# Optimization experiments

Measured on AMD Instinct MI355X. Metric: run time of the kernel, lower is better.

## Reference

```python
import jax, jax.numpy as jnp
import numpy as np

B, T, V, E, U = 32, 512, 8000, 256, 512


def _lstm(x, mask, Wk, Wr, b):
    """Keras-semantics masked LSTM. x:[B,T,D], mask:[B,T] bool -> [B,T,U].
    At masked steps the state is not updated and the output carries the
    previous hidden state (Keras K.rnn default, zero_output_for_mask=False)."""
    xW = jnp.einsum('btd,dk->btk', x, Wk) + b  # precompute input projections [B,T,4U]
    units = Wr.shape[0]

    def step(carry, inp):
        h, c = carry
        xw, m = inp  # xw:[B,4U], m:[B]
        z = xw + h @ Wr
        i, f, g, o = jnp.split(z, 4, axis=-1)  # Keras gate order i,f,c,o
        c_new = jax.nn.sigmoid(f) * c + jax.nn.sigmoid(i) * jnp.tanh(g)
        h_new = jax.nn.sigmoid(o) * jnp.tanh(c_new)
        m2 = m[:, None]
        h_new = jnp.where(m2, h_new, h)
        c_new = jnp.where(m2, c_new, c)
        return (h_new, c_new), h_new

    h0 = jnp.zeros((x.shape[0], units), x.dtype)
    _, ys = jax.lax.scan(step, (h0, h0), (jnp.swapaxes(xW, 0, 1), mask.T))
    return jnp.swapaxes(ys, 0, 1)


def _bidir(x, mask, kf, rf, bf, kb, rb, bb):
    fwd = _lstm(x, mask, kf, rf, bf)
    bwd = _lstm(x[:, ::-1], mask[:, ::-1], kb, rb, bb)[:, ::-1]
    return jnp.concatenate([fwd, bwd], axis=-1)


def setup_inputs() -> dict:
    key = jax.random.key(0)
    ks = jax.random.split(key, 12)
    s = 0.05  # glorot-ish scale for stability through tanh/sigmoid
    return {
        'tokens': jax.random.randint(ks[0], (B, T), 0, V, dtype=jnp.int32),
        'emb': jax.random.normal(ks[1], (V, E), jnp.float32) * s,
        'k1f': jax.random.normal(ks[2], (E, 4 * U), jnp.float32) * s,
        'r1f': jax.random.normal(ks[3], (U, 4 * U), jnp.float32) * s,
        'b1f': jnp.zeros((4 * U,), jnp.float32),
        'k1b': jax.random.normal(ks[4], (E, 4 * U), jnp.float32) * s,
        'r1b': jax.random.normal(ks[5], (U, 4 * U), jnp.float32) * s,
        'b1b': jnp.zeros((4 * U,), jnp.float32),
        'k2f': jax.random.normal(ks[6], (2 * U, 4 * U), jnp.float32) * s,
        'r2f': jax.random.normal(ks[7], (U, 4 * U), jnp.float32) * s,
        'b2f': jnp.zeros((4 * U,), jnp.float32),
        'k2b': jax.random.normal(ks[8], (2 * U, 4 * U), jnp.float32) * s,
        'r2b': jax.random.normal(ks[9], (U, 4 * U), jnp.float32) * s,
        'b2b': jnp.zeros((4 * U,), jnp.float32),
        'wd': jax.random.normal(ks[10], (2 * U, V), jnp.float32) * s,
        'bd': jnp.zeros((V,), jnp.float32),
    }


def reference(tokens, emb, k1f, r1f, b1f, k1b, r1b, b1b,
              k2f, r2f, b2f, k2b, r2b, b2b, wd, bd):
    mask = tokens != 0  # Embedding(mask_zero=True)
    x = emb[tokens]  # [B,T,E]
    h1 = _bidir(x, mask, k1f, r1f, b1f, k1b, r1b, b1b)  # [B,T,2U]; Dropout is identity at inference
    h2 = _bidir(h1, mask, k2f, r2f, b2f, k2b, r2b, b2b)  # [B,T,2U]
    logits = jnp.einsum('btd,dv->btv', h2, wd) + bd  # [B,T,V]
    return logits
```

## Files before the change

### kernel.cpp

```cpp
#include <hip/hip_runtime.h>
#include <hip/hip_bf16.h>
#include <stdint.h>

#define B_   32
#define T_   512
#define V_   8000
#define E_   256
#define U_   512
#define BT_  (B_*T_)
#define G4_  (4*U_)
#define GWG  32
#define UPW  (U_/GWG)

typedef unsigned short ushort_t;
typedef __attribute__((ext_vector_type(8))) short   short8;
typedef __attribute__((ext_vector_type(4))) float   floatx4;

__device__ __forceinline__ float bf2f(ushort_t u) {
    union { unsigned int i; float f; } v; v.i = ((unsigned int)u) << 16; return v.f;
}
__device__ __forceinline__ ushort_t f2bf(float f) {
    union { float f; unsigned int i; } v; v.f = f;
    unsigned int r = v.i + 0x7fffu + ((v.i >> 16) & 1u);
    return (ushort_t)(r >> 16);
}
__device__ __forceinline__ float sigmoidf_(float x) { return 1.0f / (1.0f + __expf(-x)); }
__device__ __forceinline__ float tanhf_(float x) {
    float ax = fabsf(x);
    float e  = __expf(-2.0f * ax);
    float r  = (1.0f - e) / (1.0f + e);
    return copysignf(r, x);
}

__device__ __forceinline__ void stg_h_sc1(ushort_t* p, unsigned int v) {
    asm volatile("global_store_short %0, %1, off sc0 sc1"
                 :: "v"(p), "v"(v) : "memory");
}
template<int OFFB>
__device__ __forceinline__ short8 ldg_h_sc1(const ushort_t* p) {
    short8 r;
    asm volatile("global_load_dwordx4 %0, %1, off offset:%2 sc0 sc1"
                 : "=&v"(r) : "v"(p), "i"(OFFB));
    return r;
}

__global__ void embed_kernel(const int* __restrict__ tokens,
                             const float* __restrict__ emb,
                             ushort_t* __restrict__ x)
{
    int row = blockIdx.x * 4 + (threadIdx.x >> 6);
    int col = (threadIdx.x & 63) * 4;
    int tok = tokens[row];
    const float4 v = *(const float4*)(emb + (size_t)tok * E_ + col);
    ushort_t* dst = x + (size_t)row * E_ + col;
    dst[0] = f2bf(v.x); dst[1] = f2bf(v.y); dst[2] = f2bf(v.z); dst[3] = f2bf(v.w);
}

__global__ void transpose_f32_bf16(const float* __restrict__ in,
                                   ushort_t* __restrict__ out, int R, int C)
{
    __shared__ ushort_t tile[32][33];
    int c0 = blockIdx.x * 32, r0 = blockIdx.y * 32;
    int r = threadIdx.x >> 3;
    int c4 = (threadIdx.x & 7) * 4;
    const float* src = in + (size_t)(r0 + r) * C + c0 + c4;
    #pragma unroll
    for (int i = 0; i < 4; ++i) tile[r][c4 + i] = f2bf(src[i]);
    __syncthreads();
    ushort_t* dst = out + (size_t)(c0 + r) * R + r0 + c4;
    #pragma unroll
    for (int i = 0; i < 4; ++i) dst[i] = tile[c4 + i][r];
}

template <int MODE>
__global__ __launch_bounds__(256)
void gemm_bt(const ushort_t* __restrict__ A,
             const ushort_t* __restrict__ BT,
             const float* __restrict__ bias,
             void* __restrict__ Cv,
             int M, int Nd, int K)
{
    const int tid = threadIdx.x, lane = tid & 63, wave = tid >> 6;
    const int wm = wave >> 1, wn = wave & 1;
    const int m0 = blockIdx.x * 128;
    const int n0 = blockIdx.y * 128;
    __shared__ __align__(16) ushort_t As[128 * 32];
    __shared__ __align__(16) ushort_t Bs[128 * 32];
    floatx4 acc[4][4];
    #pragma unroll
    for (int i = 0; i < 4; ++i)
        #pragma unroll
        for (int j = 0; j < 4; ++j) acc[i][j] = (floatx4){0.f, 0.f, 0.f, 0.f};

    const int lr = lane >> 2;
    const int lk = (lane & 3) * 8;
    const int rowL = wave * 32 + lr;
    const int ra0 = m0 + rowL;
    int rb0 = n0 + rowL;      if (rb0 > Nd - 1) rb0 = Nd - 1;
    int rb1 = n0 + rowL + 16; if (rb1 > Nd - 1) rb1 = Nd - 1;

    for (int k0 = 0; k0 < K; k0 += 32) {
        uint4 a0 = *(const uint4*)(A  + (size_t)ra0        * K + k0 + lk);
        uint4 a1 = *(const uint4*)(A  + (size_t)(ra0 + 16) * K + k0 + lk);
        uint4 b0 = *(const uint4*)(BT + (size_t)rb0        * K + k0 + lk);
        uint4 b1 = *(const uint4*)(BT + (size_t)rb1        * K + k0 + lk);
        __syncthreads();
        *(uint4*)(As + (rowL     ) * 32 + lk) = a0;
        *(uint4*)(As + (rowL + 16) * 32 + lk) = a1;
        *(uint4*)(Bs + (rowL     ) * 32 + lk) = b0;
        *(uint4*)(Bs + (rowL + 16) * 32 + lk) = b1;
        __syncthreads();
        short8 af[4], bw[4];
        #pragma unroll
        for (int i = 0; i < 4; ++i)
            af[i] = *(const short8*)(As + (wm * 64 + i * 16 + (lane & 15)) * 32 + (lane >> 4) * 8);
        #pragma unroll
        for (int j = 0; j < 4; ++j)
            bw[j] = *(const short8*)(Bs + (wn * 64 + j * 16 + (lane & 15)) * 32 + (lane >> 4) * 8);
        #pragma unroll
        for (int i = 0; i < 4; ++i)
            #pragma unroll
            for (int j = 0; j < 4; ++j)
                acc[i][j] = __builtin_amdgcn_mfma_f32_16x16x32_bf16(af[i], bw[j], acc[i][j], 0, 0, 0);
    }
    #pragma unroll
    for (int j = 0; j < 4; ++j) {
        int n = n0 + wn * 64 + j * 16 + (lane & 15);
        bool nok = (n < Nd);
        float bv = nok ? bias[nok ? n : 0] : 0.f;
        #pragma unroll
        for (int i = 0; i < 4; ++i) {
            #pragma unroll
            for (int r = 0; r < 4; ++r) {
                int m = m0 + wm * 64 + i * 16 + (lane >> 4) * 4 + r;
                if (nok) {
                    float v = acc[i][j][r] + bv;
                    if (MODE == 1) {
                        ((float*)Cv)[(size_t)m * Nd + n] = v;
                    } else if (MODE == 0) {
                        ((ushort_t*)Cv)[(size_t)m * Nd + n] = f2bf(v);
                    } else {
                        int t    = m & (T_ - 1);
                        int b    = m >> 9;
                        int gate = n >> 9;
                        int u    = n & 511;
                        int g    = u >> 4;
                        int u16  = u & 15;
                        size_t dst = (size_t)t * 65536 + g * 2048 + b * 64 + u16 * 4 + gate;
                        ((ushort_t*)Cv)[dst] = f2bf(v);
                    }
                }
            }
        }
    }
}

__global__ __launch_bounds__(512)
void lstm_rec(const ushort_t* __restrict__ xw,
              const ushort_t* __restrict__ WrTf,
              const ushort_t* __restrict__ WrTb,
              const int* __restrict__ tokens,
              ushort_t* __restrict__ h,
              int* __restrict__ flg)
{
    const int tid  = threadIdx.x;
    const int lane = tid & 63;
    const int wave = tid >> 6;
    const int dir  = blockIdx.y;
    const int g    = blockIdx.x;
    const int mt   = wave >> 2;
    const int q    = wave & 3;
    const int l16  = lane & 15;
    const int l4   = lane >> 4;
    const ushort_t* WrT = dir ? WrTb : WrTf;

    short8 bfrag[16];
    {
        const ushort_t* src = WrT + (size_t)(q * U_ + g * UPW + l16) * U_ + l4 * 8;
        #pragma unroll
        for (int kb = 0; kb < 16; ++kb) bfrag[kb] = *(const short8*)(src + kb * 32);
    }

    __shared__ float zs[4][32][17];

    const int b_me = tid >> 4;
    const int u_me = tid & 15;
    const int u_g  = g * UPW + u_me;
    float c_st = 0.0f, h_st = 0.0f;
    const ushort_t* xbase = xw + (size_t)dir * BT_ * G4_
                          + (size_t)g * 2048 + (size_t)b_me * 64 + u_me * 4;
    const int* fpoll = &flg[dir * GWG + (lane & 31)];
    int* fmine = &flg[dir * GWG + g];

    for (int s = 0; s < T_; ++s) {
        const int t = dir ? (T_ - 1 - s) : s;
        ushort4 xv = *(const ushort4*)(xbase + (size_t)t * 65536);
        int tok = tokens[b_me * T_ + t];

        floatx4 acc;
        if (s > 0) {
            while (true) {
                int v = __hip_atomic_load(fpoll, __ATOMIC_RELAXED,
                                          __HIP_MEMORY_SCOPE_AGENT);
                if (__ballot(v >= s) == ~0ull) break;
            }
            __builtin_amdgcn_sched_barrier(0);
            const int tp = dir ? (t + 1) : (t - 1);
            const ushort_t* hp = h + ((size_t)(mt * 16 + l16) * T_ + tp) * (2 * U_)
                                   + dir * U_ + l4 * 8;
            short8 af[16];
            af[0]  = ldg_h_sc1< 0 * 64>(hp);
            af[1]  = ldg_h_sc1< 1 * 64>(hp);
            af[2]  = ldg_h_sc1< 2 * 64>(hp);
            af[3]  = ldg_h_sc1< 3 * 64>(hp);
            af[4]  = ldg_h_sc1< 4 * 64>(hp);
            af[5]  = ldg_h_sc1< 5 * 64>(hp);
            af[6]  = ldg_h_sc1< 6 * 64>(hp);
            af[7]  = ldg_h_sc1< 7 * 64>(hp);
            af[8]  = ldg_h_sc1< 8 * 64>(hp);
            af[9]  = ldg_h_sc1< 9 * 64>(hp);
            af[10] = ldg_h_sc1<10 * 64>(hp);
            af[11] = ldg_h_sc1<11 * 64>(hp);
            af[12] = ldg_h_sc1<12 * 64>(hp);
            af[13] = ldg_h_sc1<13 * 64>(hp);
            af[14] = ldg_h_sc1<14 * 64>(hp);
            af[15] = ldg_h_sc1<15 * 64>(hp);
            asm volatile("s_waitcnt vmcnt(0)" ::: "memory");
            __builtin_amdgcn_sched_barrier(0);
            floatx4 a0 = (floatx4){0.f,0.f,0.f,0.f}, a1 = a0, a2 = a0, a3 = a0;
            #pragma unroll
            for (int kb = 0; kb < 16; kb += 4) {
                a0 = __builtin_amdgcn_mfma_f32_16x16x32_bf16(af[kb    ], bfrag[kb    ], a0, 0, 0, 0);
                a1 = __builtin_amdgcn_mfma_f32_16x16x32_bf16(af[kb + 1], bfrag[kb + 1], a1, 0, 0, 0);
                a2 = __builtin_amdgcn_mfma_f32_16x16x32_bf16(af[kb + 2], bfrag[kb + 2], a2, 0, 0, 0);
                a3 = __builtin_amdgcn_mfma_f32_16x16x32_bf16(af[kb + 3], bfrag[kb + 3], a3, 0, 0, 0);
            }
            acc = (a0 + a1) + (a2 + a3);
        } else {
            acc = (floatx4){0.f, 0.f, 0.f, 0.f};
        }
        #pragma unroll
        for (int r = 0; r < 4; ++r)
            zs[q][mt * 16 + l4 * 4 + r][l16] = acc[r];
        asm volatile("s_waitcnt lgkmcnt(0)" ::: "memory");
        __builtin_amdgcn_s_barrier();
        __builtin_amdgcn_sched_barrier(0);

        float zi = bf2f(xv.x) + zs[0][b_me][u_me];
        float zf = bf2f(xv.y) + zs[1][b_me][u_me];
        float zg = bf2f(xv.z) + zs[2][b_me][u_me];
        float zo = bf2f(xv.w) + zs[3][b_me][u_me];
        float c_new = sigmoidf_(zf) * c_st + sigmoidf_(zi) * tanhf_(zg);
        float h_new = sigmoidf_(zo) * tanhf_(c_new);
        bool msk = (tok != 0);
        float h_sel = msk ? h_new : h_st;
        float c_sel = msk ? c_new : c_st;
        h_st = h_sel; c_st = c_sel;
        stg_h_sc1(h + ((size_t)b_me * T_ + t) * (2 * U_) + dir * U_ + u_g,
                  (unsigned int)f2bf(h_sel));
        asm volatile("s_waitcnt vmcnt(0)" ::: "memory");
        __builtin_amdgcn_s_barrier();
        __builtin_amdgcn_sched_barrier(0);
        if (tid == 0)
            __hip_atomic_store(fmine, s + 1, __ATOMIC_RELAXED,
                               __HIP_MEMORY_SCOPE_AGENT);
    }
}

extern "C" void kernel_launch(void* const* d_in, const int* in_sizes, int n_in,
                              void* d_out, int out_size, void* d_ws, size_t ws_size,
                              hipStream_t stream)
{
    const int*   tokens = (const int*)d_in[0];
    const float* emb  = (const float*)d_in[1];
    const float* k1f  = (const float*)d_in[2];
    const float* r1f  = (const float*)d_in[3];
    const float* b1f  = (const float*)d_in[4];
    const float* k1b  = (const float*)d_in[5];
    const float* r1b  = (const float*)d_in[6];
    const float* b1b  = (const float*)d_in[7];
    const float* k2f  = (const float*)d_in[8];
    const float* r2f  = (const float*)d_in[9];
    const float* b2f  = (const float*)d_in[10];
    const float* k2b  = (const float*)d_in[11];
    const float* r2b  = (const float*)d_in[12];
    const float* b2b  = (const float*)d_in[13];
    const float* wd   = (const float*)d_in[14];
    const float* bd   = (const float*)d_in[15];
    float* out = (float*)d_out;

    const size_t MB = 1024 * 1024;
    ushort_t* xw   = (ushort_t*)d_out;
    ushort_t* x    = (ushort_t*)((char*)d_out + 128 * MB);
    ushort_t* h1   = (ushort_t*)((char*)d_out + 136 * MB);
    char* wb       = (char*)d_out + 168 * MB;
    ushort_t* k1fT = (ushort_t*)(wb);
    ushort_t* k1bT = (ushort_t*)(wb + 1  * MB);
    ushort_t* k2fT = (ushort_t*)(wb + 2  * MB);
    ushort_t* k2bT = (ushort_t*)(wb + 6  * MB);
    ushort_t* r1fT = (ushort_t*)(wb + 10 * MB);
    ushort_t* r1bT = (ushort_t*)(wb + 12 * MB);
    ushort_t* r2fT = (ushort_t*)(wb + 14 * MB);
    ushort_t* r2bT = (ushort_t*)(wb + 16 * MB);
    int*      flg  = (int*)d_ws;
    ushort_t* h2   = (ushort_t*)((char*)d_ws + 65536);
    ushort_t* wdT  = (ushort_t*)((char*)d_ws + 65536 + (size_t)BT_ * 2 * U_ * 2);

    hipMemsetAsync(flg, 0, 2 * 2 * T_ * sizeof(int), stream);
    embed_kernel<<<BT_ / 4, 256, 0, stream>>>(tokens, emb, x);

    transpose_f32_bf16<<<dim3(2048/32, 256/32 ), 256, 0, stream>>>(k1f, k1fT, 256,  2048);
    transpose_f32_bf16<<<dim3(2048/32, 256/32 ), 256, 0, stream>>>(k1b, k1bT, 256,  2048);
    transpose_f32_bf16<<<dim3(2048/32, 1024/32), 256, 0, stream>>>(k2f, k2fT, 1024, 2048);
    transpose_f32_bf16<<<dim3(2048/32, 1024/32), 256, 0, stream>>>(k2b, k2bT, 1024, 2048);
    transpose_f32_bf16<<<dim3(2048/32, 512/32 ), 256, 0, stream>>>(r1f, r1fT, 512,  2048);
    transpose_f32_bf16<<<dim3(2048/32, 512/32 ), 256, 0, stream>>>(r1b, r1bT, 512,  2048);
    transpose_f32_bf16<<<dim3(2048/32, 512/32 ), 256, 0, stream>>>(r2f, r2fT, 512,  2048);
    transpose_f32_bf16<<<dim3(2048/32, 512/32 ), 256, 0, stream>>>(r2b, r2bT, 512,  2048);
    transpose_f32_bf16<<<dim3(8000/32, 1024/32), 256, 0, stream>>>(wd,  wdT,  1024, 8000);

    gemm_bt<2><<<dim3(128, 16), 256, 0, stream>>>(x, k1fT, b1f, xw,                      BT_, G4_, E_);
    gemm_bt<2><<<dim3(128, 16), 256, 0, stream>>>(x, k1bT, b1b, xw + (size_t)BT_ * G4_,  BT_, G4_, E_);
    lstm_rec<<<dim3(GWG, 2), 512, 0, stream>>>(xw, r1fT, r1bT, tokens, h1, flg);
    gemm_bt<2><<<dim3(128, 16), 256, 0, stream>>>(h1, k2fT, b2f, xw,                     BT_, G4_, 2*U_);
    gemm_bt<2><<<dim3(128, 16), 256, 0, stream>>>(h1, k2bT, b2b, xw + (size_t)BT_ * G4_, BT_, G4_, 2*U_);
    lstm_rec<<<dim3(GWG, 2), 512, 0, stream>>>(xw, r2fT, r2bT, tokens, h2, flg + 2 * GWG);
    gemm_bt<1><<<dim3(128, (V_ + 127) / 128), 256, 0, stream>>>(h2, wdT, bd, out, BT_, V_, 2*U_);
}
```

Before: 7.253 ms.

## Replace flag-based inter-block sync with sentinel-polled hidden state data

```diff
diff --git a/kernel.cpp b/kernel.cpp
--- a/kernel.cpp
+++ b/kernel.cpp
@@ -11,10 +11,12 @@
 #define G4_  (4*U_)
 #define GWG  32
 #define UPW  (U_/GWG)
+#define SENT_ 0x7F7F7F7Fu
 
 typedef unsigned short ushort_t;
-typedef __attribute__((ext_vector_type(8))) short   short8;
-typedef __attribute__((ext_vector_type(4))) float   floatx4;
+typedef __attribute__((ext_vector_type(8))) short        short8;
+typedef __attribute__((ext_vector_type(4))) float        floatx4;
+typedef __attribute__((ext_vector_type(4))) unsigned int uint4v;
 
 __device__ __forceinline__ float bf2f(ushort_t u) {
     union { unsigned int i; float f; } v; v.i = ((unsigned int)u) << 16; return v.f;
@@ -32,8 +34,8 @@
     return copysignf(r, x);
 }
 
-__device__ __forceinline__ void stg_h_sc1(ushort_t* p, unsigned int v) {
-    asm volatile("global_store_short %0, %1, off sc0 sc1"
+__device__ __forceinline__ void stg_h_sc1_d(ushort_t* p, unsigned int v) {
+    asm volatile("global_store_dword %0, %1, off sc0 sc1"
                  :: "v"(p), "v"(v) : "memory");
 }
 template<int OFFB>
@@ -160,8 +162,7 @@
               const ushort_t* __restrict__ WrTf,
               const ushort_t* __restrict__ WrTb,
               const int* __restrict__ tokens,
-              ushort_t* __restrict__ h,
-              int* __restrict__ flg)
+              ushort_t* __restrict__ h)
 {
     const int tid  = threadIdx.x;
     const int lane = tid & 63;
@@ -189,8 +190,6 @@
     float c_st = 0.0f, h_st = 0.0f;
     const ushort_t* xbase = xw + (size_t)dir * BT_ * G4_
                           + (size_t)g * 2048 + (size_t)b_me * 64 + u_me * 4;
-    const int* fpoll = &flg[dir * GWG + (lane & 31)];
-    int* fmine = &flg[dir * GWG + g];
 
     for (int s = 0; s < T_; ++s) {
         const int t = dir ? (T_ - 1 - s) : s;
@@ -199,33 +198,38 @@
 
         floatx4 acc;
         if (s > 0) {
-            while (true) {
-                int v = __hip_atomic_load(fpoll, __ATOMIC_RELAXED,
-                                          __HIP_MEMORY_SCOPE_AGENT);
-                if (__ballot(v >= s) == ~0ull) break;
-            }
-            __builtin_amdgcn_sched_barrier(0);
             const int tp = dir ? (t + 1) : (t - 1);
             const ushort_t* hp = h + ((size_t)(mt * 16 + l16) * T_ + tp) * (2 * U_)
                                    + dir * U_ + l4 * 8;
             short8 af[16];
-            af[0]  = ldg_h_sc1< 0 * 64>(hp);
-            af[1]  = ldg_h_sc1< 1 * 64>(hp);
-            af[2]  = ldg_h_sc1< 2 * 64>(hp);
-            af[3]  = ldg_h_sc1< 3 * 64>(hp);
-            af[4]  = ldg_h_sc1< 4 * 64>(hp);
-            af[5]  = ldg_h_sc1< 5 * 64>(hp);
-            af[6]  = ldg_h_sc1< 6 * 64>(hp);
-            af[7]  = ldg_h_sc1< 7 * 64>(hp);
-            af[8]  = ldg_h_sc1< 8 * 64>(hp);
-            af[9]  = ldg_h_sc1< 9 * 64>(hp);
-            af[10] = ldg_h_sc1<10 * 64>(hp);
-            af[11] = ldg_h_sc1<11 * 64>(hp);
-            af[12] = ldg_h_sc1<12 * 64>(hp);
-            af[13] = ldg_h_sc1<13 * 64>(hp);
-            af[14] = ldg_h_sc1<14 * 64>(hp);
-            af[15] = ldg_h_sc1<15 * 64>(hp);
-            asm volatile("s_waitcnt vmcnt(0)" ::: "memory");
+            while (true) {
+                af[0]  = ldg_h_sc1< 0 * 64>(hp);
+                af[1]  = ldg_h_sc1< 1 * 64>(hp);
+                af[2]  = ldg_h_sc1< 2 * 64>(hp);
+                af[3]  = ldg_h_sc1< 3 * 64>(hp);
+                af[4]  = ldg_h_sc1< 4 * 64>(hp);
+                af[5]  = ldg_h_sc1< 5 * 64>(hp);
+                af[6]  = ldg_h_sc1< 6 * 64>(hp);
+                af[7]  = ldg_h_sc1< 7 * 64>(hp);
+                af[8]  = ldg_h_sc1< 8 * 64>(hp);
+                af[9]  = ldg_h_sc1< 9 * 64>(hp);
+                af[10] = ldg_h_sc1<10 * 64>(hp);
+                af[11] = ldg_h_sc1<11 * 64>(hp);
+                af[12] = ldg_h_sc1<12 * 64>(hp);
+                af[13] = ldg_h_sc1<13 * 64>(hp);
+                af[14] = ldg_h_sc1<14 * 64>(hp);
+                af[15] = ldg_h_sc1<15 * 64>(hp);
+                asm volatile("s_waitcnt vmcnt(0)" ::: "memory");
+                __builtin_amdgcn_sched_barrier(0);
+                unsigned int bad = 0u;
+                #pragma unroll
+                for (int kb = 0; kb < 16; ++kb) {
+                    uint4v d = __builtin_bit_cast(uint4v, af[kb]);
+                    bad |= (unsigned int)((d.x == SENT_) | (d.y == SENT_) |
+                                          (d.z == SENT_) | (d.w == SENT_));
+                }
+                if (__ballot(bad == 0u) == ~0ull) break;
+            }
             __builtin_amdgcn_sched_barrier(0);
             floatx4 a0 = (floatx4){0.f,0.f,0.f,0.f}, a1 = a0, a2 = a0, a3 = a0;
             #pragma unroll
@@ -246,24 +250,30 @@
         __builtin_amdgcn_s_barrier();
         __builtin_amdgcn_sched_barrier(0);
 
-        float zi = bf2f(xv.x) + zs[0][b_me][u_me];
-        float zf = bf2f(xv.y) + zs[1][b_me][u_me];
-        float zg = bf2f(xv.z) + zs[2][b_me][u_me];
-        float zo = bf2f(xv.w) + zs[3][b_me][u_me];
+        float zi_s = zs[0][b_me][u_me];
+        float zf_s = zs[1][b_me][u_me];
+        float zg_s = zs[2][b_me][u_me];
+        float zo_s = zs[3][b_me][u_me];
+        asm volatile("s_waitcnt lgkmcnt(0)" ::: "memory");
+        __builtin_amdgcn_s_barrier();
+        __builtin_amdgcn_sched_barrier(0);
+
+        float zi = bf2f(xv.x) + zi_s;
+        float zf = bf2f(xv.y) + zf_s;
+        float zg = bf2f(xv.z) + zg_s;
+        float zo = bf2f(xv.w) + zo_s;
         float c_new = sigmoidf_(zf) * c_st + sigmoidf_(zi) * tanhf_(zg);
         float h_new = sigmoidf_(zo) * tanhf_(c_new);
         bool msk = (tok != 0);
         float h_sel = msk ? h_new : h_st;
         float c_sel = msk ? c_new : c_st;
         h_st = h_sel; c_st = c_sel;
-        stg_h_sc1(h + ((size_t)b_me * T_ + t) * (2 * U_) + dir * U_ + u_g,
-                  (unsigned int)f2bf(h_sel));
-        asm volatile("s_waitcnt vmcnt(0)" ::: "memory");
-        __builtin_amdgcn_s_barrier();
-        __builtin_amdgcn_sched_barrier(0);
-        if (tid == 0)
-            __hip_atomic_store(fmine, s + 1, __ATOMIC_RELAXED,
-                               __HIP_MEMORY_SCOPE_AGENT);
+        unsigned int hb = (unsigned int)f2bf(h_sel);
+        unsigned int pb = (unsigned int)__shfl_xor((int)hb, 1);
+        if (!(u_me & 1)) {
+            ushort_t* hw = h + ((size_t)b_me * T_ + t) * (2 * U_) + dir * U_ + u_g;
+            stg_h_sc1_d(hw, hb | (pb << 16));
+        }
     }
 }
 
@@ -302,11 +312,11 @@
     ushort_t* r1bT = (ushort_t*)(wb + 12 * MB);
     ushort_t* r2fT = (ushort_t*)(wb + 14 * MB);
     ushort_t* r2bT = (ushort_t*)(wb + 16 * MB);
-    int*      flg  = (int*)d_ws;
     ushort_t* h2   = (ushort_t*)((char*)d_ws + 65536);
     ushort_t* wdT  = (ushort_t*)((char*)d_ws + 65536 + (size_t)BT_ * 2 * U_ * 2);
 
-    hipMemsetAsync(flg, 0, 2 * 2 * T_ * sizeof(int), stream);
+    hipMemsetAsync(h1, 0x7F, (size_t)BT_ * 2 * U_ * 2, stream);
+    hipMemsetAsync(h2, 0x7F, (size_t)BT_ * 2 * U_ * 2, stream);
     embed_kernel<<<BT_ / 4, 256, 0, stream>>>(tokens, emb, x);
 
     transpose_f32_bf16<<<dim3(2048/32, 256/32 ), 256, 0, stream>>>(k1f, k1fT, 256,  2048);
@@ -321,9 +331,9 @@
 
     gemm_bt<2><<<dim3(128, 16), 256, 0, stream>>>(x, k1fT, b1f, xw,                      BT_, G4_, E_);
     gemm_bt<2><<<dim3(128, 16), 256, 0, stream>>>(x, k1bT, b1b, xw + (size_t)BT_ * G4_,  BT_, G4_, E_);
-    lstm_rec<<<dim3(GWG, 2), 512, 0, stream>>>(xw, r1fT, r1bT, tokens, h1, flg);
+    lstm_rec<<<dim3(GWG, 2), 512, 0, stream>>>(xw, r1fT, r1bT, tokens, h1);
     gemm_bt<2><<<dim3(128, 16), 256, 0, stream>>>(h1, k2fT, b2f, xw,                     BT_, G4_, 2*U_);
     gemm_bt<2><<<dim3(128, 16), 256, 0, stream>>>(h1, k2bT, b2b, xw + (size_t)BT_ * G4_, BT_, G4_, 2*U_);
-    lstm_rec<<<dim3(GWG, 2), 512, 0, stream>>>(xw, r2fT, r2bT, tokens, h2, flg + 2 * GWG);
+    lstm_rec<<<dim3(GWG, 2), 512, 0, stream>>>(xw, r2fT, r2bT, tokens, h2);
     gemm_bt<1><<<dim3(128, (V_ + 127) / 128), 256, 0, stream>>>(h2, wdT, bd, out, BT_, V_, 2*U_);
 }
```

New measurement: 8.755 ms. 20.7% more time.
